# Kernel optimization log

Measured on AMD Instinct MI355X. Metric: run time of the kernel, lower is better.

The kernel has to match this reference:

```python
import jax, jax.numpy as jnp
import numpy as np

V, E, H, B, S, L = 32000, 512, 1024, 128, 256, 2


def setup_inputs() -> dict:
    key = jax.random.key(0)
    ks = jax.random.split(key, 20)
    sc = 0.02
    n = lambda k, shape: jax.random.normal(k, shape, dtype=jnp.float32) * sc
    return {
        "input_ids": jax.random.randint(ks[0], (B,), 0, V),
        "h0": jax.random.normal(ks[1], (L, B, H), dtype=jnp.float32),
        "c0": jax.random.normal(ks[2], (L, B, H), dtype=jnp.float32),
        "enc_out": jax.random.normal(ks[3], (S, B, H), dtype=jnp.float32),
        "emb": n(ks[4], (V, E)),
        "w_ih0": n(ks[5], (4 * H, E)),
        "w_hh0": n(ks[6], (4 * H, H)),
        "b_ih0": n(ks[7], (4 * H,)),
        "b_hh0": n(ks[8], (4 * H,)),
        "w_ih1": n(ks[9], (4 * H, H)),
        "w_hh1": n(ks[10], (4 * H, H)),
        "b_ih1": n(ks[11], (4 * H,)),
        "b_hh1": n(ks[12], (4 * H,)),
        "attn_w": n(ks[13], (H, H)),
        "attn_b": n(ks[14], (H,)),
        "concat_w": n(ks[15], (H, 2 * H)),
        "concat_b": n(ks[16], (H,)),
        "out_w": n(ks[17], (V, H)),
        "out_b": n(ks[18], (V,)),
    }


def _lstm_step(x, h, c, w_ih, w_hh, b_ih, b_hh):
    # PyTorch gate order: i, f, g, o
    g = x @ w_ih.T + b_ih + h @ w_hh.T + b_hh  # [B, 4H]
    i, f, gg, o = jnp.split(g, 4, axis=-1)
    c_new = jax.nn.sigmoid(f) * c + jax.nn.sigmoid(i) * jnp.tanh(gg)
    h_new = jax.nn.sigmoid(o) * jnp.tanh(c_new)
    return h_new, c_new


def reference(input_ids, h0, c0, enc_out, emb, w_ih0, w_hh0, b_ih0, b_hh0,
              w_ih1, w_hh1, b_ih1, b_hh1, attn_w, attn_b, concat_w, concat_b,
              out_w, out_b):
    x = emb[input_ids]  # [B, E] (dropout is identity in eval)
    h_0, c_0 = _lstm_step(x, h0[0], c0[0], w_ih0, w_hh0, b_ih0, b_hh0)
    h_1, c_1 = _lstm_step(h_0, h0[1], c0[1], w_ih1, w_hh1, b_ih1, b_hh1)
    rnn_out = h_1  # [B, H] == rnn_output.squeeze(0)
    # Luong general attention: scores[b,s] = <W enc[s,b], rnn_out[b]>
    e_proj = enc_out @ attn_w.T + attn_b          # [S, B, H]
    scores = jnp.einsum('sbh,bh->bs', e_proj, rnn_out)  # [B, S]
    attn = jax.nn.softmax(scores, axis=-1)
    context = jnp.einsum('bs,sbh->bh', attn, enc_out)   # [B, H]
    concat_out = jnp.tanh(
        jnp.concatenate([rnn_out, context], axis=-1) @ concat_w.T + concat_b)
    logits = concat_out @ out_w.T + out_b         # [B, V]
    h_new = jnp.stack([h_0, h_1])
    c_new = jnp.stack([c_0, c_1])
    return logits, h_new, c_new
```

## Files before the change

kernel.cpp:

```cpp
#include <hip/hip_runtime.h>
#include <hip/hip_bf16.h>
#include <cstddef>
#include <cstdint>

constexpr int Bv = 128;
constexpr int Sv = 256;
constexpr int Hv = 1024;
constexpr int Ev = 512;
constexpr int Vv = 32000;

typedef __attribute__((ext_vector_type(4))) float f32x4;
typedef __attribute__((ext_vector_type(8))) short short8;

__device__ __forceinline__ uint2 cvt4(float4 v) {
  union { __hip_bfloat162 b; unsigned u; } lo, hi;
  lo.b = __float22bfloat162_rn(float2{v.x, v.y});
  hi.b = __float22bfloat162_rn(float2{v.z, v.w});
  uint2 r;
  r.x = lo.u;
  r.y = hi.u;
  return r;
}
__device__ __forceinline__ unsigned short cvt1(float x) {
  union { __hip_bfloat16 b; unsigned short u; } c;
  c.b = __float2bfloat16(x);
  return c.u;
}

template <int BM, int BN, int BK, int SPLIT, int WTR, int GATHER, int MINW>
__global__ __launch_bounds__(256, MINW) void gemm_mfma(
    const int* __restrict__ ids,
    const float* __restrict__ A1, int lda1, int K1,
    const float* __restrict__ A2, int lda2, int K2,
    const float* __restrict__ W1, int ldw1,
    const float* __restrict__ W2, int ldw2,
    const float* __restrict__ bias1, const float* __restrict__ bias2,
    float* __restrict__ C, int ldc, int N) {
  constexpr int LP = BK + 8;
  constexpr int KQ = BK / 4;
  constexpr int KSUB = BK / 32;
  constexpr int WAVES_N = (BN >= 64) ? 2 : 1;
  constexpr int WAVES_M = 4 / WAVES_N;
  constexpr int WM = BM / WAVES_M;
  constexpr int FM = WM / 16;
  constexpr int FN = BN / (16 * WAVES_N);
  constexpr int WN = FN * 16;
  constexpr int ACH = (BM * BK) / (4 * 256);
  constexpr int WCH = (BN * BK) / (4 * 256);
  constexpr int WVN = WTR ? (BK * 8 / 256) : WCH;

  __shared__ unsigned short Al[BM * LP];
  __shared__ unsigned short Wl[BN * LP];

  const int tid = threadIdx.x;
  const int wid = tid >> 6, lane = tid & 63;
  const int nBlock = blockIdx.x * BN;
  const int mBlock = blockIdx.y * BM;
  const int z = blockIdx.z;
  int wm, wn;
  if (WAVES_N == 2) { wm = (wid >> 1) * WM; wn = (wid & 1) * WN; }
  else              { wm = wid * WM;        wn = 0; }

  float4 av[ACH], wv[WVN];

  auto load_tile = [&](int kg) {
    const bool seg1 = kg < K1;
    const float* Wseg = seg1 ? W1 : W2;
    const int ldw = seg1 ? ldw1 : ldw2;
    const int kloc = seg1 ? kg : kg - K1;
#pragma unroll
    for (int i = 0; i < ACH; i++) {
      int c = tid + i * 256;
      int m = c / KQ, kq = (c % KQ) * 4;
      const float* arow;
      if (seg1) {
        if (GATHER) arow = A1 + (size_t)ids[mBlock + m] * lda1;
        else        arow = A1 + (size_t)(mBlock + m) * lda1;
      } else {
        arow = A2 + (size_t)(mBlock + m) * lda2;
      }
      av[i] = *(const float4*)(arow + kloc + kq);
    }
    if (WTR) {
#pragma unroll
      for (int i = 0; i < WVN; i++) {
        int c = tid + i * 256;
        int row = c >> 3, colq = c & 7;
        wv[i] = *(const float4*)(Wseg + (size_t)(kloc + row) * ldw + nBlock + colq * 4);
      }
    } else {
#pragma unroll
      for (int i = 0; i < WCH; i++) {
        int c = tid + i * 256;
        int n = c / KQ, kq = (c % KQ) * 4;
        wv[i] = *(const float4*)(Wseg + (size_t)(nBlock + n) * ldw + kloc + kq);
      }
    }
  };

  const int KT = K1 + K2;
  const int KS = KT / SPLIT;
  const int kbeg = z * KS;
  const int NS = KS / BK;
  load_tile(kbeg);
  f32x4 acc[FM][FN] = {};

  for (int step = 0; step < NS; ++step) {
    __syncthreads();
#pragma unroll
    for (int i = 0; i < ACH; i++) {
      int c = tid + i * 256;
      int m = c / KQ, kq = (c % KQ) * 4;
      *(uint2*)&Al[m * LP + kq] = cvt4(av[i]);
    }
    if (WTR) {
#pragma unroll
      for (int i = 0; i < WVN; i++) {
        int c = tid + i * 256;
        int row = c >> 3, colq = c & 7;
        Wl[(colq * 4 + 0) * LP + row] = cvt1(wv[i].x);
        Wl[(colq * 4 + 1) * LP + row] = cvt1(wv[i].y);
        Wl[(colq * 4 + 2) * LP + row] = cvt1(wv[i].z);
        Wl[(colq * 4 + 3) * LP + row] = cvt1(wv[i].w);
      }
    } else {
#pragma unroll
      for (int i = 0; i < WCH; i++) {
        int c = tid + i * 256;
        int n = c / KQ, kq = (c % KQ) * 4;
        *(uint2*)&Wl[n * LP + kq] = cvt4(wv[i]);
      }
    }
    __syncthreads();

    if (step + 1 < NS) load_tile(kbeg + (step + 1) * BK);

    const int klane = (lane >> 4) << 3;
    const int r = lane & 15;
    short8 af[KSUB][FM], wf[KSUB][FN];
#pragma unroll
    for (int ks = 0; ks < KSUB; ks++) {
#pragma unroll
      for (int f = 0; f < FM; f++)
        af[ks][f] = *(const short8*)&Al[(wm + f * 16 + r) * LP + ks * 32 + klane];
#pragma unroll
      for (int f = 0; f < FN; f++)
        wf[ks][f] = *(const short8*)&Wl[(wn + f * 16 + r) * LP + ks * 32 + klane];
    }
#pragma unroll
    for (int ks = 0; ks < KSUB; ks++)
#pragma unroll
      for (int fm = 0; fm < FM; fm++)
#pragma unroll
        for (int fn = 0; fn < FN; fn++)
          acc[fm][fn] = __builtin_amdgcn_mfma_f32_16x16x32_bf16(
              af[ks][fm], wf[ks][fn], acc[fm][fn], 0, 0, 0);
  }

  float* Cp = C + (size_t)z * gridDim.y * BM * ldc;
  const int col = lane & 15, rb = (lane >> 4) << 2;
#pragma unroll
  for (int fn = 0; fn < FN; fn++) {
    int n = nBlock + wn + fn * 16 + col;
    float bsum = 0.f;
    if (z == 0) {
      if (bias1) bsum += bias1[n];
      if (bias2) bsum += bias2[n];
    }
#pragma unroll
    for (int fm = 0; fm < FM; fm++) {
#pragma unroll
      for (int j = 0; j < 4; j++) {
        int m = mBlock + wm + fm * 16 + rb + j;
        Cp[(size_t)m * ldc + n] = acc[fm][fn][j] + bsum;
      }
    }
  }
}

template <int P>
__global__ void lstm_pw(const float* __restrict__ Gp,
                        const float* __restrict__ c_prev,
                        float* __restrict__ h_out,
                        float* __restrict__ c_out) {
  int i4 = blockIdx.x * 256 + threadIdx.x;
  int b = i4 >> 8, j4 = i4 & 255;
  float4 gi{}, gf{}, gg{}, go{};
#pragma unroll
  for (int p = 0; p < P; p++) {
    const float4* g = (const float4*)(Gp + (size_t)p * Bv * 4 * Hv + (size_t)b * 4096);
    float4 a = g[j4], bb = g[256 + j4], c = g[512 + j4], d = g[768 + j4];
    gi.x += a.x; gi.y += a.y; gi.z += a.z; gi.w += a.w;
    gf.x += bb.x; gf.y += bb.y; gf.z += bb.z; gf.w += bb.w;
    gg.x += c.x; gg.y += c.y; gg.z += c.z; gg.w += c.w;
    go.x += d.x; go.y += d.y; go.z += d.z; go.w += d.w;
  }
  float4 c4 = ((const float4*)c_prev)[i4];
  float4 h4, cn4;
  float* gip = &gi.x; float* gfp = &gf.x; float* ggp = &gg.x; float* gop = &go.x;
  float* cp = &c4.x; float* hp = &h4.x; float* cnp = &cn4.x;
#pragma unroll
  for (int u = 0; u < 4; u++) {
    float si = 1.f / (1.f + expf(-gip[u]));
    float sf = 1.f / (1.f + expf(-gfp[u]));
    float so = 1.f / (1.f + expf(-gop[u]));
    float cn = sf * cp[u] + si * tanhf(ggp[u]);
    hp[u] = so * tanhf(cn);
    cnp[u] = cn;
  }
  ((float4*)h_out)[i4] = h4;
  ((float4*)c_out)[i4] = cn4;
}

__global__ __launch_bounds__(256) void attn_part(
    const float* __restrict__ enc, const float* __restrict__ qp,
    float* __restrict__ numb, float2* __restrict__ mden) {
  const int b = blockIdx.x, ch = blockIdx.y;
  const int t = threadIdx.x, lane = t & 63, wid = t >> 6;
  const int sbase = ch * 64;
  __shared__ float qs[1024];
  __shared__ float es[64];
  {
    const float4* q0 = (const float4*)(qp + (size_t)b * Hv);
    const float4* q1 = (const float4*)(qp + 1 * Bv * Hv + (size_t)b * Hv);
    const float4* q2 = (const float4*)(qp + 2 * Bv * Hv + (size_t)b * Hv);
    const float4* q3 = (const float4*)(qp + 3 * Bv * Hv + (size_t)b * Hv);
    float4 a = q0[t], bq = q1[t], c = q2[t], d = q3[t];
    float4 s;
    s.x = a.x + bq.x + c.x + d.x; s.y = a.y + bq.y + c.y + d.y;
    s.z = a.z + bq.z + c.z + d.z; s.w = a.w + bq.w + c.w + d.w;
    ((float4*)qs)[t] = s;
  }
  __syncthreads();

  const float4* q4 = (const float4*)qs;
  for (int i = 0; i < 16; i++) {
    int s = sbase + wid * 16 + i;
    const float4* e4 = (const float4*)(enc + ((size_t)s * Bv + b) * Hv);
    float sum = 0.f;
#pragma unroll
    for (int j = 0; j < 4; j++) {
      int idx = lane + j * 64;
      float4 e = e4[idx], qq = q4[idx];
      sum += e.x * qq.x + e.y * qq.y + e.z * qq.z + e.w * qq.w;
    }
#pragma unroll
    for (int o = 32; o; o >>= 1) sum += __shfl_xor(sum, o);
    if (lane == 0) es[wid * 16 + i] = sum;
  }
  __syncthreads();

  if (wid == 0) {
    float v = es[lane];
    float m = v;
#pragma unroll
    for (int o = 32; o; o >>= 1) m = fmaxf(m, __shfl_xor(m, o));
    float e = expf(v - m);
    float den = e;
#pragma unroll
    for (int o = 32; o; o >>= 1) den += __shfl_xor(den, o);
    es[lane] = e;
    if (lane == 0) mden[b * 4 + ch] = make_float2(m, den);
  }
  __syncthreads();

  float4 acc = make_float4(0.f, 0.f, 0.f, 0.f);
  const float* ebase = enc + ((size_t)sbase * Bv + b) * Hv + t * 4;
#pragma unroll 4
  for (int s = 0; s < 64; s++) {
    float4 e = *(const float4*)(ebase + (size_t)s * Bv * Hv);
    float w = es[s];
    acc.x += w * e.x; acc.y += w * e.y; acc.z += w * e.z; acc.w += w * e.w;
  }
  *(float4*)(numb + ((size_t)ch * Bv + b) * Hv + t * 4) = acc;
}

__global__ __launch_bounds__(256) void attn_fin(
    const float* __restrict__ numb, const float2* __restrict__ mden,
    float* __restrict__ ctx) {
  const int b = blockIdx.x, t = threadIdx.x;
  float2 md0 = mden[b * 4 + 0], md1 = mden[b * 4 + 1];
  float2 md2 = mden[b * 4 + 2], md3 = mden[b * 4 + 3];
  float M = fmaxf(fmaxf(md0.x, md1.x), fmaxf(md2.x, md3.x));
  float s0 = expf(md0.x - M), s1 = expf(md1.x - M);
  float s2 = expf(md2.x - M), s3 = expf(md3.x - M);
  float inv = 1.f / (s0 * md0.y + s1 * md1.y + s2 * md2.y + s3 * md3.y);
  const float4* n0 = (const float4*)(numb + (size_t)b * Hv);
  const float4* n1 = (const float4*)(numb + 1 * (size_t)Bv * Hv + (size_t)b * Hv);
  const float4* n2 = (const float4*)(numb + 2 * (size_t)Bv * Hv + (size_t)b * Hv);
  const float4* n3 = (const float4*)(numb + 3 * (size_t)Bv * Hv + (size_t)b * Hv);
  float4 a = n0[t], bb = n1[t], c = n2[t], d = n3[t];
  float4 r;
  r.x = (s0 * a.x + s1 * bb.x + s2 * c.x + s3 * d.x) * inv;
  r.y = (s0 * a.y + s1 * bb.y + s2 * c.y + s3 * d.y) * inv;
  r.z = (s0 * a.z + s1 * bb.z + s2 * c.z + s3 * d.z) * inv;
  r.w = (s0 * a.w + s1 * bb.w + s2 * c.w + s3 * d.w) * inv;
  ((float4*)(ctx + (size_t)b * Hv))[t] = r;
}

__global__ void finish_cat(const float* __restrict__ catp,
                           float* __restrict__ cat) {
  int i4 = blockIdx.x * 256 + threadIdx.x;
  constexpr int ST = Bv * Hv / 4;
  const float4* p = (const float4*)catp;
  float4 a = p[i4], b = p[ST + i4], c = p[2 * ST + i4], d = p[3 * ST + i4];
  float4 r;
  r.x = tanhf(a.x + b.x + c.x + d.x);
  r.y = tanhf(a.y + b.y + c.y + d.y);
  r.z = tanhf(a.z + b.z + c.z + d.z);
  r.w = tanhf(a.w + b.w + c.w + d.w);
  ((float4*)cat)[i4] = r;
}

extern "C" void kernel_launch(void* const* d_in, const int* in_sizes, int n_in,
                              void* d_out, int out_size, void* d_ws,
                              size_t ws_size, hipStream_t stream) {
  const int*   ids      = (const int*)d_in[0];
  const float* h0       = (const float*)d_in[1];
  const float* c0       = (const float*)d_in[2];
  const float* enc      = (const float*)d_in[3];
  const float* emb      = (const float*)d_in[4];
  const float* w_ih0    = (const float*)d_in[5];
  const float* w_hh0    = (const float*)d_in[6];
  const float* b_ih0    = (const float*)d_in[7];
  const float* b_hh0    = (const float*)d_in[8];
  const float* w_ih1    = (const float*)d_in[9];
  const float* w_hh1    = (const float*)d_in[10];
  const float* b_ih1    = (const float*)d_in[11];
  const float* b_hh1    = (const float*)d_in[12];
  const float* attn_w   = (const float*)d_in[13];
  const float* attn_b   = (const float*)d_in[14];
  const float* concat_w = (const float*)d_in[15];
  const float* concat_b = (const float*)d_in[16];
  const float* out_w    = (const float*)d_in[17];
  const float* out_b    = (const float*)d_in[18];
  (void)attn_b;

  float* logits = (float*)d_out;
  float* hout   = logits + (size_t)Bv * Vv;
  float* cout   = hout + 2 * Bv * Hv;

  float* ws   = (float*)d_ws;
  float* G0p  = ws;
  float* G1p  = G0p + 3 * 524288;
  float* qp   = G1p + 4 * (size_t)524288;
  float* catp = qp + 4 * 131072;
  float* cat  = catp + 4 * 131072;
  float* ctx  = cat + 131072;
  float* numb = G0p;
  float2* mden = (float2*)(G0p + 524288);

  const float* h_b = hout + Bv * Hv;

  gemm_mfma<64, 32, 64, 3, 0, 1, 4><<<dim3(128, 2, 3), 256, 0, stream>>>(
      ids, emb, Ev, Ev, h0, Hv, Hv, w_ih0, Ev, w_hh0, Hv, b_ih0, b_hh0,
      G0p, 4 * Hv, 4 * Hv);
  lstm_pw<3><<<128, 256, 0, stream>>>(G0p, c0, hout, cout);
  gemm_mfma<64, 32, 64, 4, 0, 0, 4><<<dim3(128, 2, 4), 256, 0, stream>>>(
      nullptr, hout, Hv, Hv, h0 + Bv * Hv, Hv, Hv, w_ih1, Hv, w_hh1, Hv,
      b_ih1, b_hh1, G1p, 4 * Hv, 4 * Hv);
  lstm_pw<4><<<128, 256, 0, stream>>>(G1p, c0 + Bv * Hv, hout + Bv * Hv,
                                      cout + Bv * Hv);
  gemm_mfma<64, 32, 64, 4, 1, 0, 4><<<dim3(32, 2, 4), 256, 0, stream>>>(
      nullptr, h_b, Hv, Hv, nullptr, 0, 0, attn_w, Hv,
      nullptr, 0, nullptr, nullptr, qp, Hv, Hv);
  attn_part<<<dim3(128, 4), 256, 0, stream>>>(enc, qp, numb, mden);
  attn_fin<<<128, 256, 0, stream>>>(numb, mden, ctx);
  gemm_mfma<64, 32, 64, 4, 0, 0, 4><<<dim3(32, 2, 4), 256, 0, stream>>>(
      nullptr, h_b, Hv, Hv, ctx, Hv, Hv, concat_w, 2 * Hv,
      concat_w + Hv, 2 * Hv, concat_b, nullptr, catp, Hv, Hv);
  finish_cat<<<128, 256, 0, stream>>>(catp, cat);
  gemm_mfma<128, 128, 64, 1, 0, 0, 1><<<dim3(250, 1, 1), 256, 0, stream>>>(
      nullptr, cat, Hv, Hv, nullptr, 0, 0, out_w, Hv, nullptr, 0,
      out_b, nullptr, logits, Vv, Vv);
}
```

Measured before the change: 159.3 us.

## Split attention over sixteen sequence chunks instead of four

Splits the attention partial kernel into 16 chunks of 16 sequence positions rather than 4 chunks of 64, growing the grid from 512 to 2048 blocks so more CUs stream the 128 MB encoder tensor in parallel. The per-chunk softmax now uses a simple shared-memory max/sum. The finalize kernel combines 16 partials with a numb layout indexed by batch then chunk. Workspace pointers move numb to G1p to fit the larger partial buffer. The cost is more partial writes and reads in the finalize step.

```diff
diff --git a/kernel.cpp b/kernel.cpp
--- a/kernel.cpp
+++ b/kernel.cpp
@@ -217,9 +217,9 @@
     float* __restrict__ numb, float2* __restrict__ mden) {
   const int b = blockIdx.x, ch = blockIdx.y;
   const int t = threadIdx.x, lane = t & 63, wid = t >> 6;
-  const int sbase = ch * 64;
+  const int sbase = ch * 16;
   __shared__ float qs[1024];
-  __shared__ float es[64];
+  __shared__ float es[16], ee[16];
   {
     const float4* q0 = (const float4*)(qp + (size_t)b * Hv);
     const float4* q1 = (const float4*)(qp + 1 * Bv * Hv + (size_t)b * Hv);
@@ -234,9 +234,10 @@
   __syncthreads();
 
   const float4* q4 = (const float4*)qs;
-  for (int i = 0; i < 16; i++) {
-    int s = sbase + wid * 16 + i;
-    const float4* e4 = (const float4*)(enc + ((size_t)s * Bv + b) * Hv);
+#pragma unroll
+  for (int i = 0; i < 4; i++) {
+    int sl = wid * 4 + i;
+    const float4* e4 = (const float4*)(enc + ((size_t)(sbase + sl) * Bv + b) * Hv);
     float sum = 0.f;
 #pragma unroll
     for (int j = 0; j < 4; j++) {
@@ -246,56 +247,61 @@
     }
 #pragma unroll
     for (int o = 32; o; o >>= 1) sum += __shfl_xor(sum, o);
-    if (lane == 0) es[wid * 16 + i] = sum;
+    if (lane == 0) es[sl] = sum;
   }
   __syncthreads();
 
-  if (wid == 0) {
-    float v = es[lane];
-    float m = v;
-#pragma unroll
-    for (int o = 32; o; o >>= 1) m = fmaxf(m, __shfl_xor(m, o));
-    float e = expf(v - m);
-    float den = e;
-#pragma unroll
-    for (int o = 32; o; o >>= 1) den += __shfl_xor(den, o);
-    es[lane] = e;
-    if (lane == 0) mden[b * 4 + ch] = make_float2(m, den);
-  }
+  float m = es[0];
+#pragma unroll
+  for (int i = 1; i < 16; i++) m = fmaxf(m, es[i]);
+  if (t < 16) ee[t] = expf(es[t] - m);
   __syncthreads();
+  if (t == 0) {
+    float den = 0.f;
+#pragma unroll
+    for (int i = 0; i < 16; i++) den += ee[i];
+    mden[b * 16 + ch] = make_float2(m, den);
+  }
 
   float4 acc = make_float4(0.f, 0.f, 0.f, 0.f);
   const float* ebase = enc + ((size_t)sbase * Bv + b) * Hv + t * 4;
-#pragma unroll 4
-  for (int s = 0; s < 64; s++) {
+#pragma unroll
+  for (int s = 0; s < 16; s++) {
     float4 e = *(const float4*)(ebase + (size_t)s * Bv * Hv);
-    float w = es[s];
+    float w = ee[s];
     acc.x += w * e.x; acc.y += w * e.y; acc.z += w * e.z; acc.w += w * e.w;
   }
-  *(float4*)(numb + ((size_t)ch * Bv + b) * Hv + t * 4) = acc;
+  *(float4*)(numb + ((size_t)b * 16 + ch) * Hv + t * 4) = acc;
 }
 
 __global__ __launch_bounds__(256) void attn_fin(
     const float* __restrict__ numb, const float2* __restrict__ mden,
     float* __restrict__ ctx) {
   const int b = blockIdx.x, t = threadIdx.x;
-  float2 md0 = mden[b * 4 + 0], md1 = mden[b * 4 + 1];
-  float2 md2 = mden[b * 4 + 2], md3 = mden[b * 4 + 3];
-  float M = fmaxf(fmaxf(md0.x, md1.x), fmaxf(md2.x, md3.x));
-  float s0 = expf(md0.x - M), s1 = expf(md1.x - M);
-  float s2 = expf(md2.x - M), s3 = expf(md3.x - M);
-  float inv = 1.f / (s0 * md0.y + s1 * md1.y + s2 * md2.y + s3 * md3.y);
-  const float4* n0 = (const float4*)(numb + (size_t)b * Hv);
-  const float4* n1 = (const float4*)(numb + 1 * (size_t)Bv * Hv + (size_t)b * Hv);
-  const float4* n2 = (const float4*)(numb + 2 * (size_t)Bv * Hv + (size_t)b * Hv);
-  const float4* n3 = (const float4*)(numb + 3 * (size_t)Bv * Hv + (size_t)b * Hv);
-  float4 a = n0[t], bb = n1[t], c = n2[t], d = n3[t];
-  float4 r;
-  r.x = (s0 * a.x + s1 * bb.x + s2 * c.x + s3 * d.x) * inv;
-  r.y = (s0 * a.y + s1 * bb.y + s2 * c.y + s3 * d.y) * inv;
-  r.z = (s0 * a.z + s1 * bb.z + s2 * c.z + s3 * d.z) * inv;
-  r.w = (s0 * a.w + s1 * bb.w + s2 * c.w + s3 * d.w) * inv;
-  ((float4*)(ctx + (size_t)b * Hv))[t] = r;
+  float mv[16], dv[16];
+  float M = -3.4e38f;
+#pragma unroll
+  for (int c = 0; c < 16; c++) {
+    float2 md = mden[b * 16 + c];
+    mv[c] = md.x; dv[c] = md.y;
+    M = fmaxf(M, md.x);
+  }
+  float den = 0.f, sc[16];
+#pragma unroll
+  for (int c = 0; c < 16; c++) {
+    sc[c] = expf(mv[c] - M);
+    den += sc[c] * dv[c];
+  }
+  float inv = 1.f / den;
+  float4 r = make_float4(0.f, 0.f, 0.f, 0.f);
+#pragma unroll
+  for (int c = 0; c < 16; c++) {
+    float4 n = *(const float4*)(numb + ((size_t)b * 16 + c) * Hv + t * 4);
+    float s = sc[c];
+    r.x += s * n.x; r.y += s * n.y; r.z += s * n.z; r.w += s * n.w;
+  }
+  r.x *= inv; r.y *= inv; r.z *= inv; r.w *= inv;
+  *(float4*)(ctx + (size_t)b * Hv + t * 4) = r;
 }
 
 __global__ void finish_cat(const float* __restrict__ catp,
@@ -347,8 +353,8 @@
   float* catp = qp + 4 * 131072;
   float* cat  = catp + 4 * 131072;
   float* ctx  = cat + 131072;
-  float* numb = G0p;
-  float2* mden = (float2*)(G0p + 524288);
+  float* numb = G1p;
+  float2* mden = (float2*)G0p;
 
   const float* h_b = hout + Bv * Hv;
 
@@ -364,7 +370,7 @@
   gemm_mfma<64, 32, 64, 4, 1, 0, 4><<<dim3(32, 2, 4), 256, 0, stream>>>(
       nullptr, h_b, Hv, Hv, nullptr, 0, 0, attn_w, Hv,
       nullptr, 0, nullptr, nullptr, qp, Hv, Hv);
-  attn_part<<<dim3(128, 4), 256, 0, stream>>>(enc, qp, numb, mden);
+  attn_part<<<dim3(128, 16), 256, 0, stream>>>(enc, qp, numb, mden);
   attn_fin<<<128, 256, 0, stream>>>(numb, mden, ctx);
   gemm_mfma<64, 32, 64, 4, 0, 0, 4><<<dim3(32, 2, 4), 256, 0, stream>>>(
       nullptr, h_b, Hv, Hv, ctx, Hv, Hv, concat_w, 2 * Hv,
```

Result: faster. 150.8 us (-5.3%).
